# Optimization experiments

Measured on AMD Instinct MI355X. Metric: run time of the kernel, lower is better.

The kernel has to match this reference:

```python
import jax, jax.numpy as jnp
import numpy as np

B, S, D, H, DFF = 2, 4096, 512, 8, 2048
DK = D // H
EPS = 1e-5


def layer_norm(x, g, b):
    mu = jnp.mean(x, axis=-1, keepdims=True)
    var = jnp.mean((x - mu) ** 2, axis=-1, keepdims=True)
    return (x - mu) * jax.lax.rsqrt(var + EPS) * g + b


def setup_inputs() -> dict:
    key = jax.random.key(0)
    ks = jax.random.split(key, 12)
    s = 1.0 / np.sqrt(D)
    return {
        "x": jax.random.normal(ks[0], (B, S, D), jnp.float32),
        "mask": jnp.ones((B, 1, 1, S), jnp.int32),
        "wq": jax.random.normal(ks[1], (D, D), jnp.float32) * s,
        "wk": jax.random.normal(ks[2], (D, D), jnp.float32) * s,
        "wv": jax.random.normal(ks[3], (D, D), jnp.float32) * s,
        "wo": jax.random.normal(ks[4], (D, D), jnp.float32) * s,
        "w1": jax.random.normal(ks[5], (D, DFF), jnp.float32) * s,
        "b1": jnp.zeros((DFF,), jnp.float32),
        "w2": jax.random.normal(ks[6], (DFF, D), jnp.float32) * (1.0 / np.sqrt(DFF)),
        "b2": jnp.zeros((D,), jnp.float32),
        "g1": jnp.ones((D,), jnp.float32),
        "be1": jnp.zeros((D,), jnp.float32),
        "g2": jnp.ones((D,), jnp.float32),
        "be2": jnp.zeros((D,), jnp.float32),
    }


def reference(x, mask, wq, wk, wv, wo, w1, b1, w2, b2, g1, be1, g2, be2):
    # projections -> [B, H, S, DK]
    def split_heads(t):
        return t.reshape(B, S, H, DK).transpose(0, 2, 1, 3)

    q = split_heads(x @ wq)
    k = split_heads(x @ wk)
    v = split_heads(x @ wv)

    scores = jnp.einsum("bhqd,bhkd->bhqk", q, k) / np.sqrt(DK)
    scores = jnp.where(mask == 0, -1e9, scores)
    attn = jax.nn.softmax(scores, axis=-1)  # dropout=0 (eval)
    ctx = jnp.einsum("bhqk,bhkd->bhqd", attn, v)
    ctx = ctx.transpose(0, 2, 1, 3).reshape(B, S, D)
    attn_out = ctx @ wo

    x1 = layer_norm(x + attn_out, g1, be1)
    ff = jax.nn.relu(x1 @ w1 + b1) @ w2 + b2
    return layer_norm(x1 + ff, g2, be2)
```

## Files before the change

### kernel.cpp

```cpp
#include <hip/hip_runtime.h>
#include <hip/hip_bf16.h>


typedef unsigned short u16;
typedef unsigned int u32;
typedef __attribute__((ext_vector_type(2))) u32 u32x2;
typedef __attribute__((ext_vector_type(4))) u16 u16x4;
typedef __attribute__((ext_vector_type(8))) u16 u16x8;
typedef __attribute__((ext_vector_type(2))) float f32x2;
typedef __attribute__((ext_vector_type(4))) float f32x4;
typedef __attribute__((ext_vector_type(16))) float f32x16;
typedef __attribute__((ext_vector_type(8))) short bf16x8;

#define CB 2
#define CS 4096
#define CD 512
#define CH 8
#define CDK 64
#define CDFF 2048
#define NXC ((size_t)CB * CS * CD)
#define NSP 2
#define BH (CB * CH)
#define BHS (BH * CS)

__device__ __forceinline__ float bf2f(u16 u) {
    union { u32 i; float f; } c;
    c.i = ((u32)u) << 16;
    return c.f;
}

__device__ __forceinline__ u16 f2bf(float f) {
    u32 x = __float_as_uint(f);
    u32 r = (x + 0x7fffu + ((x >> 16) & 1u)) >> 16;
    return (u16)r;
}

__device__ __forceinline__ u32 packbf2(float a, float b) {
    __hip_bfloat162 h = __float22bfloat162_rn(float2{a, b});
    union { __hip_bfloat162 h; u32 u; } c;
    c.h = h;
    return c.u;
}

__device__ __forceinline__ void dma16(const u16* g, u16* l) {
    __builtin_amdgcn_global_load_lds(
        (const __attribute__((address_space(1))) void*)g,
        (__attribute__((address_space(3))) void*)l, 16, 0, 0);
}

__global__ void detect_dtype(const u32* __restrict__ xw, int* __restrict__ flag) {
    __shared__ int red[256];
    int sane = 0;
    for (int i = threadIdx.x; i < 2048; i += 256) {
        u32 w = xw[i];
        u32 lo = w & 0xFFFFu;
        u32 e = (lo >> 7) & 0xFFu;
        if (lo == 0u || lo == 0x8000u || (e >= 96u && e <= 159u)) sane++;
    }
    red[threadIdx.x] = sane;
    __syncthreads();
    for (int s = 128; s > 0; s >>= 1) {
        if ((int)threadIdx.x < s) red[threadIdx.x] += red[threadIdx.x + s];
        __syncthreads();
    }
    if (threadIdx.x == 0) *flag = (red[0] >= 1843) ? 1 : 0;
}

__global__ __launch_bounds__(256) void convert_bf16(
    const void* __restrict__ src, u16* __restrict__ dst, int n,
    const int* __restrict__ flag)
{
    const bool isbf = (*flag != 0);
    const int n8 = n >> 3;
    int i = blockIdx.x * 256 + threadIdx.x;
    const int stride = gridDim.x * 256;
    if (isbf) {
        const u16x8* s = (const u16x8*)src;
        u16x8* d = (u16x8*)dst;
        for (; i < n8; i += stride) d[i] = s[i];
    } else {
        const f32x4* s = (const f32x4*)src;
        for (; i < n8; i += stride) {
            f32x4 a = s[2 * i];
            f32x4 b = s[2 * i + 1];
            u16x8 o;
#pragma unroll
            for (int e = 0; e < 4; e++) {
                o[e] = f2bf(a[e]);
                o[4 + e] = f2bf(b[e]);
            }
            *(u16x8*)&dst[(size_t)i * 8] = o;
        }
    }
    if (blockIdx.x == 0 && threadIdx.x == 0) {
        for (int r = n8 * 8; r < n; r++) {
            if (isbf) dst[r] = ((const u16*)src)[r];
            else dst[r] = f2bf(((const float*)src)[r]);
        }
    }
}

struct SmallConv {
    const void* src[6];
    u16* dst[6];
    int n[6];
};

__global__ __launch_bounds__(256) void convert_small(SmallConv sc, const int* __restrict__ flag) {
    const bool isbf = (*flag != 0);
    for (int t = 0; t < 6; t++) {
        for (int i = threadIdx.x; i < sc.n[t]; i += 256) {
            if (isbf) sc.dst[t][i] = ((const u16*)sc.src[t])[i];
            else sc.dst[t][i] = f2bf(((const float*)sc.src[t])[i]);
        }
    }
}

__global__ __launch_bounds__(256) void build_mask_bits(
    const int* __restrict__ mask, unsigned long long* __restrict__ bits)
{
    int w = blockIdx.x * 4 + (threadIdx.x >> 6);
    int lane = threadIdx.x & 63;
    int b = w >> 6, t = w & 63;
    int val = mask[b * CS + t * 64 + lane];
    unsigned long long bal = __ballot(val != 0);
    if (lane == 0) bits[w] = bal;
}

__global__ __launch_bounds__(256) void transpose_cvt(
    const void* __restrict__ src, u16* __restrict__ dst,
    int R, int Cc, const int* __restrict__ flag)
{
    __shared__ float t[32][33];
    const bool isbf = (*flag != 0);
    const int r0 = blockIdx.y * 32;
    const int c0 = blockIdx.x * 32;
    const int col = threadIdx.x & 31;
    const int row = threadIdx.x >> 5;
#pragma unroll
    for (int it = 0; it < 4; it++) {
        int rr = row + it * 8;
        float v;
        if (isbf) v = bf2f(((const u16*)src)[(size_t)(r0 + rr) * Cc + c0 + col]);
        else v = ((const float*)src)[(size_t)(r0 + rr) * Cc + c0 + col];
        t[rr][col] = v;
    }
    __syncthreads();
#pragma unroll
    for (int it = 0; it < 4; it++) {
        int rr = row + it * 8;
        dst[(size_t)(c0 + rr) * R + r0 + col] = f2bf(t[col][rr]);
    }
}

#define F_SPLIT 1
#define F_BIAS  2
#define F_RELU  4

template <int FLAGS>
__global__ __launch_bounds__(256, 3) void gemm_mfma(
    const u16* __restrict__ A, const u16* __restrict__ Bt,
    const u16* __restrict__ bias, u16* __restrict__ C,
    int M, int N, int K)
{
    __shared__ u16 Asb[4096];
    __shared__ u16 Bsb[4096];

    const int tid = threadIdx.x;
    const int lane = tid & 63;
    const int wave = tid >> 6;
    const int lrow = lane & 15;
    const int quad = lane >> 4;
    const int wm = wave & 1;
    const int wn = wave >> 1;
    const int m0 = blockIdx.y * 128;
    const int n0 = blockIdx.x * 128;

    const int idx0 = wave * 128 + lane;
    const int idx1 = idx0 + 64;
    const u16* Ap0 = A + (size_t)(m0 + (idx0 >> 2)) * K + (idx0 & 3) * 8;
    const u16* Ap1 = A + (size_t)(m0 + (idx1 >> 2)) * K + (idx1 & 3) * 8;
    const u16* Bp0 = Bt + (size_t)(n0 + (idx0 >> 2)) * K + (idx0 & 3) * 8;
    const u16* Bp1 = Bt + (size_t)(n0 + (idx1 >> 2)) * K + (idx1 & 3) * 8;
    u16* Al0 = &Asb[wave * 1024];
    u16* Al1 = &Asb[wave * 1024 + 512];
    u16* Bl0 = &Bsb[wave * 1024];
    u16* Bl1 = &Bsb[wave * 1024 + 512];

    f32x4 acc[4][4];
#pragma unroll
    for (int i = 0; i < 4; i++)
#pragma unroll
        for (int j = 0; j < 4; j++) acc[i][j] = f32x4{0.f, 0.f, 0.f, 0.f};

    for (int k0 = 0; k0 < K; k0 += 32) {
        __syncthreads();
        dma16(Ap0 + k0, Al0);
        dma16(Ap1 + k0, Al1);
        dma16(Bp0 + k0, Bl0);
        dma16(Bp1 + k0, Bl1);
        __syncthreads();

        bf16x8 af[4], bfr[4];
#pragma unroll
        for (int i = 0; i < 4; i++)
            af[i] = *(const bf16x8*)&Asb[(wm * 64 + i * 16 + lrow) * 32 + quad * 8];
#pragma unroll
        for (int j = 0; j < 4; j++)
            bfr[j] = *(const bf16x8*)&Bsb[(wn * 64 + j * 16 + lrow) * 32 + quad * 8];
#pragma unroll
        for (int i = 0; i < 4; i++)
#pragma unroll
            for (int j = 0; j < 4; j++)
                acc[i][j] = __builtin_amdgcn_mfma_f32_16x16x32_bf16(
                    af[i], bfr[j], acc[i][j], 0, 0, 0);
    }

    const int mbase = m0 + wm * 64;
    const int nbase = n0 + wn * 64;
#pragma unroll
    for (int i = 0; i < 4; i++) {
#pragma unroll
        for (int j = 0; j < 4; j++) {
            const int n = nbase + j * 16 + lrow;
            if ((FLAGS & F_SPLIT) && ((nbase + j * 16) >> 9) == 2) {
                const int dk = n & 63;
                const int h = (n >> 6) & 7;
                const int sb = mbase + i * 16 + quad * 4;
                const int bb = sb >> 12;
                const int ss = sb & 4095;
                u16x4 ov;
#pragma unroll
                for (int r = 0; r < 4; r++) ov[r] = f2bf(acc[i][j][r]);
                *(u16x4*)&C[2 * NXC + (((size_t)(bb * CH + h)) * CDK + dk) * CS + ss] = ov;
            } else {
#pragma unroll
                for (int r = 0; r < 4; r++) {
                    const int m = mbase + i * 16 + quad * 4 + r;
                    float val = acc[i][j][r];
                    if (FLAGS & F_BIAS) val += bf2f(bias[n]);
                    if (FLAGS & F_RELU) val = fmaxf(val, 0.f);
                    if (FLAGS & F_SPLIT) {
                        const int proj = n >> 9;
                        const int d = n & 511;
                        const int h = d >> 6;
                        const int dk = d & 63;
                        const int bb = m >> 12;
                        const int ss = m & 4095;
                        C[proj * NXC + (((size_t)(bb * CH + h)) * CS + ss) * CDK + dk] = f2bf(val);
                    } else {
                        C[(size_t)m * N + n] = f2bf(val);
                    }
                }
            }
        }
    }
}

__global__ __launch_bounds__(256, 4) void mfma_attn2(
    const u16* __restrict__ Qb, const u16* __restrict__ Kb,
    const u16* __restrict__ Vt, const unsigned long long* __restrict__ bits,
    u16* __restrict__ pOT, float* __restrict__ Ls)
{
    __shared__ u16 KB[3][4096];
    __shared__ u16 VB[2][4096];

    const int tid = threadIdx.x;
    const int lane = tid & 63;
    const int wave = tid >> 6;
    const int qcol = lane & 31;
    const int hf = lane >> 5;

    const int bh = blockIdx.y;
    const int b = bh >> 3;
    const int z = blockIdx.z;
    const int q0 = blockIdx.x * 128 + wave * 32;

    const float SC = 0.125f * 1.44269504088896340736f;

    bf16x8 bq[4];
    const u16* qp = Qb + ((size_t)bh * CS + q0 + qcol) * CDK + hf * 8;
#pragma unroll
    for (int c = 0; c < 4; c++) {
        bf16x8 raw = *(const bf16x8*)(qp + c * 16);
        union { u32 u[4]; bf16x8 v; } cv;
#pragma unroll
        for (int j = 0; j < 4; j++)
            cv.u[j] = packbf2(bf2f((u16)raw[2 * j]) * SC, bf2f((u16)raw[2 * j + 1]) * SC);
        bq[c] = cv.v;
    }

    f32x4 z4 = {0.f, 0.f, 0.f, 0.f};
    asm volatile("" : "+v"(z4));
    f32x16 zero16;
#pragma unroll
    for (int i = 0; i < 16; i++) zero16[i] = z4[i & 3];

    f32x16 ot[2];
#pragma unroll
    for (int dt = 0; dt < 2; dt++)
#pragma unroll
        for (int i = 0; i < 16; i++) ot[dt][i] = 0.f;
    float lh = 0.f;

    const u16* kbase = Kb + (size_t)bh * CS * CDK;
    const u16* vbase = Vt + (size_t)bh * CDK * CS;
    const unsigned long long* bp = bits + b * 64;

    const int t0 = z * (CS / NSP);
    const int t1 = t0 + (CS / NSP);

    const int rsw = qcol & 7;
    int koff[2][4];
#pragma unroll
    for (int rt = 0; rt < 2; rt++)
#pragma unroll
        for (int c = 0; c < 4; c++)
            koff[rt][c] = ((rt * 32 + qcol) * 64 + (((2 * c + hf) ^ rsw) * 8)) * 2;
    const char* kb0 = (const char*)&KB[0][0];
    const char* vb0 = (const char*)&VB[0][0];

    const int w2 = wave * 2;

#define STAGE_K(KOFFB, t)                                                    \
    {                                                                        \
        const u16* kb_ = kbase + (size_t)(t) * CDK;                          \
        _Pragma("unroll")                                                    \
        for (int n = 0; n < 2; n++) {                                        \
            int idx = (w2 + n) * 64 + lane;                                  \
            int row = idx >> 3;                                              \
            int g = (idx & 7) ^ (row & 7);                                   \
            dma16(kb_ + row * CDK + g * 8,                                   \
                  (u16*)((char*)&KB[0][0] + (KOFFB) + (w2 + n) * 1024));     \
        }                                                                    \
    }
#define STAGE_V(P, t)                                                        \
    {                                                                        \
        const u16* vb_ = vbase + (t);                                        \
        _Pragma("unroll")                                                    \
        for (int n = 0; n < 2; n++) {                                        \
            int idx = (w2 + n) * 64 + lane;                                  \
            int row = idx >> 3;                                              \
            int g = (idx & 7) ^ (row & 7);                                   \
            dma16(vb_ + (size_t)row * CS + g * 8,                            \
                  (u16*)((char*)&VB[0][0] + (P) * 8192 + (w2 + n) * 1024));  \
        }                                                                    \
    }

#define TBODY(KROFF, VOFF, BM, MASKED, MIDSYNC)                              \
    {                                                                        \
        f32x2 racc = {0.f, 0.f};                                             \
        _Pragma("unroll")                                                    \
        for (int mt = 0; mt < 2; mt++) {                                     \
            f32x16 s;                                                        \
            _Pragma("unroll")                                                \
            for (int c = 0; c < 4; c++) {                                    \
                bf16x8 ak = *(const bf16x8*)(kb0 + (KROFF) + koff[mt][c]);   \
                s = __builtin_amdgcn_mfma_f32_32x32x16_bf16(                 \
                    ak, bq[c], (c == 0) ? zero16 : s, 0, 0, 0);              \
            }                                                                \
            if (MASKED) {                                                    \
                const unsigned long long bm_ = (BM);                         \
                if (bm_ != ~0ull) {                                          \
                    _Pragma("unroll")                                        \
                    for (int i = 0; i < 16; i++) {                           \
                        const int key = (i & 3) + 8 * (i >> 2) + 4 * hf + 32 * mt; \
                        if (!((bm_ >> key) & 1ull)) s[i] = -1e30f;           \
                    }                                                        \
                }                                                            \
            }                                                                \
            u32 pk[8];                                                       \
            _Pragma("unroll")                                                \
            for (int g = 0; g < 4; g++) {                                    \
                float p0 = __builtin_amdgcn_exp2f(s[4 * g + 0]);             \
                float p1 = __builtin_amdgcn_exp2f(s[4 * g + 1]);             \
                float p2 = __builtin_amdgcn_exp2f(s[4 * g + 2]);             \
                float p3 = __builtin_amdgcn_exp2f(s[4 * g + 3]);             \
                racc += f32x2{p0, p1};                                       \
                racc += f32x2{p2, p3};                                       \
                pk[2 * g + 0] = packbf2(p0, p1);                             \
                pk[2 * g + 1] = packbf2(p2, p3);                             \
            }                                                                \
            if (mt == 0) { MIDSYNC }                                         \
            _Pragma("unroll")                                                \
            for (int cc = 0; cc < 2; cc++) {                                 \
                u32x2 r0 = __builtin_amdgcn_permlane32_swap(                 \
                    pk[4 * cc + 0], pk[4 * cc + 2], false, false);           \
                u32x2 r1 = __builtin_amdgcn_permlane32_swap(                 \
                    pk[4 * cc + 1], pk[4 * cc + 3], false, false);           \
                union { u32 u[4]; bf16x8 v; } pf;                            \
                pf.u[0] = r0.x;                                              \
                pf.u[1] = r1.x;                                              \
                pf.u[2] = r0.y;                                              \
                pf.u[3] = r1.y;                                              \
                const int c = 2 * mt + cc;                                   \
                _Pragma("unroll")                                            \
                for (int dt = 0; dt < 2; dt++) {                             \
                    bf16x8 av = *(const bf16x8*)(vb0 + (VOFF) + koff[dt][c]); \
                    ot[dt] = __builtin_amdgcn_mfma_f32_32x32x16_bf16(        \
                        av, pf.v, ot[dt], 0, 0, 0);                          \
                }                                                            \
            }                                                                \
        }                                                                    \
        lh += racc.x + racc.y;                                               \
    }

#define FTILE(P, TT, KR, KS, DOV, DOK, TOPASM, MIDASM)                       \
    {                                                                        \
        asm volatile(TOPASM ::: "memory");                                   \
        __builtin_amdgcn_sched_barrier(0);                                   \
        __builtin_amdgcn_s_barrier();                                        \
        __builtin_amdgcn_sched_barrier(0);                                   \
        if (DOV) STAGE_V((P) ^ 1, (TT) + 64);                                \
        if (DOK) STAGE_K((KS), (TT) + 128);                                  \
        TBODY((KR), (P) * 8192, 0ull, 0,                                     \
              asm volatile(MIDASM ::: "memory");                             \
              __builtin_amdgcn_sched_barrier(0);                             \
              __builtin_amdgcn_s_barrier();                                  \
              __builtin_amdgcn_sched_barrier(0);)                            \
    }

    unsigned long long am = ~0ull;
    const int tb0 = t0 >> 6;
    for (int i = 0; i < 32; i++) am &= bp[tb0 + i];
    const bool allones = (am == ~0ull);

    if (allones) {
        STAGE_K(0, t0);
        STAGE_V(0, t0);
        STAGE_K(8192, t0 + 64);

        u32 kr = 0;
        for (int m = 0; m < 15; m++) {
            const int t = t0 + m * 128;
            const u32 kr1 = (kr == 16384u) ? 0u : kr + 8192u;
            const u32 ks0 = (kr1 == 16384u) ? 0u : kr1 + 8192u;
            FTILE(0, t, kr, ks0, 1, 1,
                  "s_waitcnt vmcnt(4)", "s_waitcnt vmcnt(6)")
            FTILE(1, t + 64, kr1, kr, 1, 1,
                  "s_waitcnt vmcnt(4)", "s_waitcnt vmcnt(6)")
            kr = ks0;
        }
        {
            const int t = t0 + 30 * 64;
            const u32 kr1 = (kr == 16384u) ? 0u : kr + 8192u;
            FTILE(0, t, kr, 0, 1, 0,
                  "s_waitcnt vmcnt(4)", "s_waitcnt vmcnt(4)")
            FTILE(1, t + 64, kr1, 0, 0, 0,
                  "s_waitcnt vmcnt(2)", "s_waitcnt vmcnt(0)")
        }
    } else {
        STAGE_K(0, t0);
        STAGE_V(0, t0);
        __syncthreads();
        for (int t = t0; t < t1; t += 64) {
            const int p = (t >> 6) & 1;
            const u32 kro = (u32)p * 8192u;
            if (t + 64 < t1) {
                STAGE_V(p ^ 1, t + 64);
                STAGE_K((p ^ 1) * 8192, t + 64);
            }
            TBODY(kro, p * 8192, bp[t >> 6], 1, ;)
            __syncthreads();
        }
    }
#undef FTILE
#undef TBODY
#undef STAGE_V
#undef STAGE_K

    u32x2 rr = __builtin_amdgcn_permlane32_swap(
        __float_as_uint(lh), __float_as_uint(lh), false, false);
    const float l = lh + __uint_as_float(hf ? rr.x : rr.y);

    const int q_lin = bh * CS + q0 + qcol;
    if (hf == 0) Ls[z * BHS + q_lin] = l;
    const size_t pbase = ((size_t)(z * BH + bh) * CDK) * CS + q0 + qcol;
#pragma unroll
    for (int dt = 0; dt < 2; dt++)
#pragma unroll
        for (int i = 0; i < 16; i++) {
            const int dk = (i & 3) + 8 * (i >> 2) + 4 * hf + 32 * dt;
            pOT[pbase + (size_t)dk * CS] = f2bf(ot[dt][i]);
        }
}

__global__ __launch_bounds__(256) void attn_combine(
    const u16* __restrict__ pOT, const float* __restrict__ Ls,
    u16* __restrict__ ctx)
{
    __shared__ float linv[64];
    __shared__ u16 T[64][72];

    const int bh = blockIdx.y;
    const int s0 = blockIdx.x * 64;
    const int b = bh >> 3, h = bh & 7;
    const int tid = threadIdx.x;

    if (tid < 64) {
        float L = 0.f;
#pragma unroll
        for (int z = 0; z < NSP; z++) L += Ls[z * BHS + bh * CS + s0 + tid];
        linv[tid] = (L > 0.f) ? 1.f / L : 0.f;
    }
    __syncthreads();

    const int dk = tid >> 2;
    const int sc = (tid & 3) * 16;
    float acc[16] = {};
#pragma unroll
    for (int z = 0; z < NSP; z++) {
        const u16* p = pOT + ((size_t)(z * BH + bh) * CDK + dk) * CS + s0 + sc;
        u16x8 v0 = *(const u16x8*)p;
        u16x8 v1 = *(const u16x8*)(p + 8);
#pragma unroll
        for (int e = 0; e < 8; e++) {
            acc[e] += bf2f(v0[e]);
            acc[8 + e] += bf2f(v1[e]);
        }
    }
#pragma unroll
    for (int e = 0; e < 16; e++)
        T[sc + e][dk] = f2bf(acc[e] * linv[sc + e]);
    __syncthreads();

    const int sr = tid >> 2;
    const int dc = (tid & 3) * 16;
    u16x8 o0, o1;
#pragma unroll
    for (int e = 0; e < 8; e++) {
        o0[e] = T[sr][dc + e];
        o1[e] = T[sr][dc + 8 + e];
    }
    u16* cp = &ctx[((size_t)b * CS + s0 + sr) * CD + h * CDK + dc];
    *(u16x8*)cp = o0;
    *(u16x8*)(cp + 8) = o1;
}

__global__ __launch_bounds__(256) void ln_kernel(
    const u16* __restrict__ xa, const u16* __restrict__ xb,
    const u16* __restrict__ g, const u16* __restrict__ be,
    u16* __restrict__ outb, float* __restrict__ outf,
    const int* __restrict__ flag)
{
    const int lane = threadIdx.x & 63;
    const int wave = threadIdx.x >> 6;
    const size_t row = (size_t)blockIdx.x * 4 + wave;
    const int c0 = lane * 8;

    u16x8 av = *(const u16x8*)(xa + row * CD + c0);
    u16x8 bv = *(const u16x8*)(xb + row * CD + c0);

    float v[8];
    float s1 = 0.f, s2 = 0.f;
#pragma unroll
    for (int e = 0; e < 8; e++) {
        v[e] = bf2f(av[e]) + bf2f(bv[e]);
        s1 += v[e];
        s2 += v[e] * v[e];
    }
#pragma unroll
    for (int off = 32; off > 0; off >>= 1) {
        s1 += __shfl_xor(s1, off, 64);
        s2 += __shfl_xor(s2, off, 64);
    }
    const float mu = s1 * (1.f / CD);
    const float var = fmaxf(s2 * (1.f / CD) - mu * mu, 0.f);
    const float r = rsqrtf(var + 1e-5f);

    u16x8 gv = *(const u16x8*)(g + c0);
    u16x8 ev = *(const u16x8*)(be + c0);
    float res[8];
#pragma unroll
    for (int e = 0; e < 8; e++)
        res[e] = (v[e] - mu) * r * bf2f(gv[e]) + bf2f(ev[e]);

    const int flg = *flag;
    const bool f32out = (outf != nullptr) && (flg == 0);
    if (f32out) {
        float4 o0 = make_float4(res[0], res[1], res[2], res[3]);
        float4 o1 = make_float4(res[4], res[5], res[6], res[7]);
        *(float4*)(outf + row * CD + c0) = o0;
        *(float4*)(outf + row * CD + c0 + 4) = o1;
    } else {
        u16x8 ov;
#pragma unroll
        for (int e = 0; e < 8; e++) ov[e] = f2bf(res[e]);
        *(u16x8*)(outb + row * CD + c0) = ov;
    }
}


extern "C" void kernel_launch(void* const* d_in, const int* in_sizes, int n_in,
                              void* d_out, int out_size, void* d_ws, size_t ws_size,
                              hipStream_t stream)
{
    const void* x_raw   = d_in[0];
    const int*  mask    = (const int*)d_in[1];
    const void* wq_raw  = d_in[2];
    const void* wk_raw  = d_in[3];
    const void* wv_raw  = d_in[4];
    const void* wo_raw  = d_in[5];
    const void* w1_raw  = d_in[6];
    const void* b1_raw  = d_in[7];
    const void* w2_raw  = d_in[8];
    const void* b2_raw  = d_in[9];
    const void* g1_raw  = d_in[10];
    const void* be1_raw = d_in[11];
    const void* g2_raw  = d_in[12];
    const void* be2_raw = d_in[13];

    const size_t NX = NXC;
    const size_t WSZ = (size_t)CD * CD;
    const size_t W1SZ = (size_t)CD * CDFF;

    u16* ws = (u16*)d_ws;
    int* flag = (int*)d_ws;
    unsigned long long* bits = (unsigned long long*)(ws + 512);
    u16* base = ws + 1024;
    u16* xc  = base;
    u16* q   = base + 1 * NX;
    u16* k   = base + 2 * NX;
    u16* v   = base + 3 * NX;
    u16* ctx = base + 4 * NX;
    u16* att = base + 5 * NX;
    u16* x1  = base + 6 * NX;
    u16* ffo = base + 7 * NX;
    u16* ffh = base + 8 * NX;
    u16* wt  = base + 12 * NX;
    u16* wqkvT = wt;
    u16* woT = wqkvT + 3 * WSZ;
    u16* w1T = woT + WSZ;
    u16* w2T = w1T + W1SZ;
    u16* b1c = w2T + W1SZ;
    u16* b2c = b1c + CDFF;
    u16* g1c = b2c + CD;
    u16* be1c = g1c + CD;
    u16* g2c = be1c + CD;
    u16* be2c = g2c + CD;
    u16* wend = be2c + CD;

    const size_t need = (size_t)(wend - ws) * sizeof(u16);
    if (ws_size < need) return;
    (void)k;

    u16* pOT = ffh;
    float* Ls = (float*)att;

    detect_dtype<<<1, 256, 0, stream>>>((const u32*)x_raw, flag);

    convert_bf16<<<1024, 256, 0, stream>>>(x_raw, xc, (int)NX, flag);
    build_mask_bits<<<32, 256, 0, stream>>>(mask, bits);

    transpose_cvt<<<dim3(CD / 32, CD / 32), 256, 0, stream>>>(wq_raw, wqkvT, CD, CD, flag);
    transpose_cvt<<<dim3(CD / 32, CD / 32), 256, 0, stream>>>(wk_raw, wqkvT + WSZ, CD, CD, flag);
    transpose_cvt<<<dim3(CD / 32, CD / 32), 256, 0, stream>>>(wv_raw, wqkvT + 2 * WSZ, CD, CD, flag);
    transpose_cvt<<<dim3(CD / 32, CD / 32), 256, 0, stream>>>(wo_raw, woT, CD, CD, flag);
    transpose_cvt<<<dim3(CDFF / 32, CD / 32), 256, 0, stream>>>(w1_raw, w1T, CD, CDFF, flag);
    transpose_cvt<<<dim3(CD / 32, CDFF / 32), 256, 0, stream>>>(w2_raw, w2T, CDFF, CD, flag);

    SmallConv sc;
    sc.src[0] = b1_raw;  sc.dst[0] = b1c;  sc.n[0] = CDFF;
    sc.src[1] = b2_raw;  sc.dst[1] = b2c;  sc.n[1] = CD;
    sc.src[2] = g1_raw;  sc.dst[2] = g1c;  sc.n[2] = CD;
    sc.src[3] = be1_raw; sc.dst[3] = be1c; sc.n[3] = CD;
    sc.src[4] = g2_raw;  sc.dst[4] = g2c;  sc.n[4] = CD;
    sc.src[5] = be2_raw; sc.dst[5] = be2c; sc.n[5] = CD;
    convert_small<<<1, 256, 0, stream>>>(sc, flag);

    const int M = CB * CS;

    gemm_mfma<F_SPLIT><<<dim3(1536 / 128, M / 128), 256, 0, stream>>>(
        xc, wqkvT, nullptr, q, M, 1536, CD);

    mfma_attn2<<<dim3(CS / 128, BH, NSP), 256, 0, stream>>>(q, k, v, bits, pOT, Ls);
    attn_combine<<<dim3(CS / 64, BH), 256, 0, stream>>>(pOT, Ls, ctx);

    gemm_mfma<0><<<dim3(CD / 128, M / 128), 256, 0, stream>>>(
        ctx, woT, nullptr, att, M, CD, CD);

    ln_kernel<<<dim3(M / 4), 256, 0, stream>>>(xc, att, g1c, be1c, x1, nullptr, flag);

    gemm_mfma<F_BIAS | F_RELU><<<dim3(CDFF / 128, M / 128), 256, 0, stream>>>(
        x1, w1T, b1c, ffh, M, CDFF, CD);
    gemm_mfma<F_BIAS><<<dim3(CD / 128, M / 128), 256, 0, stream>>>(
        ffh, w2T, b2c, ffo, M, CD, CDFF);

    ln_kernel<<<dim3(M / 4), 256, 0, stream>>>(x1, ffo, g2c, be2c,
                                               (u16*)d_out, (float*)d_out, flag);
}
```

Measured before the change: 339.2 us.

## Merge weight prep launches into one kernel and widen GEMM K-tile with swizzled LDS

The six transpose launches, the mask-bit build and the small-parameter conversion are folded into a single prep_all kernel that dispatches on block index, cutting per-launch overhead. Separately, the MFMA GEMM now stages a 64-wide K slice per iteration instead of 32, with an XOR swizzle on the 16-byte LDS chunk index. This halves the barrier count per K step and is meant to avoid LDS bank conflicts on the fragment reads. LDS per block doubles to 32 KB, which may affect occupancy at 3 blocks per CU.

```diff
diff --git a/kernel.cpp b/kernel.cpp
--- a/kernel.cpp
+++ b/kernel.cpp
@@ -100,56 +100,69 @@
     }
 }
 
-struct SmallConv {
-    const void* src[6];
-    u16* dst[6];
-    int n[6];
+struct PrepArgs {
+    const void* tsrc[6];
+    u16* tdst[6];
+    int R[6], Cc[6], nbx[6];
+    int cum[7];
+    const int* mask;
+    unsigned long long* bits;
+    const void* ssrc[6];
+    u16* sdst[6];
+    int sn[6];
 };
 
-__global__ __launch_bounds__(256) void convert_small(SmallConv sc, const int* __restrict__ flag) {
-    const bool isbf = (*flag != 0);
-    for (int t = 0; t < 6; t++) {
-        for (int i = threadIdx.x; i < sc.n[t]; i += 256) {
-            if (isbf) sc.dst[t][i] = ((const u16*)sc.src[t])[i];
-            else sc.dst[t][i] = f2bf(((const float*)sc.src[t])[i]);
-        }
-    }
-}
-
-__global__ __launch_bounds__(256) void build_mask_bits(
-    const int* __restrict__ mask, unsigned long long* __restrict__ bits)
-{
-    int w = blockIdx.x * 4 + (threadIdx.x >> 6);
-    int lane = threadIdx.x & 63;
-    int b = w >> 6, t = w & 63;
-    int val = mask[b * CS + t * 64 + lane];
-    unsigned long long bal = __ballot(val != 0);
-    if (lane == 0) bits[w] = bal;
-}
-
-__global__ __launch_bounds__(256) void transpose_cvt(
-    const void* __restrict__ src, u16* __restrict__ dst,
-    int R, int Cc, const int* __restrict__ flag)
-{
-    __shared__ float t[32][33];
-    const bool isbf = (*flag != 0);
-    const int r0 = blockIdx.y * 32;
-    const int c0 = blockIdx.x * 32;
-    const int col = threadIdx.x & 31;
-    const int row = threadIdx.x >> 5;
-#pragma unroll
-    for (int it = 0; it < 4; it++) {
-        int rr = row + it * 8;
-        float v;
-        if (isbf) v = bf2f(((const u16*)src)[(size_t)(r0 + rr) * Cc + c0 + col]);
-        else v = ((const float*)src)[(size_t)(r0 + rr) * Cc + c0 + col];
-        t[rr][col] = v;
-    }
-    __syncthreads();
-#pragma unroll
-    for (int it = 0; it < 4; it++) {
-        int rr = row + it * 8;
-        dst[(size_t)(c0 + rr) * R + r0 + col] = f2bf(t[col][rr]);
+__global__ __launch_bounds__(256) void prep_all(PrepArgs pa, const int* __restrict__ flag) {
+    const int bid = blockIdx.x;
+    const int tid = threadIdx.x;
+    if (bid < pa.cum[6]) {
+        __shared__ float t[32][33];
+        int w = 0;
+#pragma unroll
+        for (int k = 1; k < 6; k++) w += (bid >= pa.cum[k]) ? 1 : 0;
+        const int local = bid - pa.cum[w];
+        const int nbx = pa.nbx[w];
+        const int bx = local % nbx;
+        const int by = local / nbx;
+        const int R = pa.R[w];
+        const int Cc = pa.Cc[w];
+        const void* src = pa.tsrc[w];
+        u16* dst = pa.tdst[w];
+        const bool isbf = (*flag != 0);
+        const int r0 = by * 32;
+        const int c0 = bx * 32;
+        const int col = tid & 31;
+        const int row = tid >> 5;
+#pragma unroll
+        for (int it = 0; it < 4; it++) {
+            int rr = row + it * 8;
+            float v;
+            if (isbf) v = bf2f(((const u16*)src)[(size_t)(r0 + rr) * Cc + c0 + col]);
+            else v = ((const float*)src)[(size_t)(r0 + rr) * Cc + c0 + col];
+            t[rr][col] = v;
+        }
+        __syncthreads();
+#pragma unroll
+        for (int it = 0; it < 4; it++) {
+            int rr = row + it * 8;
+            dst[(size_t)(c0 + rr) * R + r0 + col] = f2bf(t[col][rr]);
+        }
+    } else if (bid < pa.cum[6] + 32) {
+        const int local = bid - pa.cum[6];
+        int w = local * 4 + (tid >> 6);
+        int lane = tid & 63;
+        int b = w >> 6, t = w & 63;
+        int val = pa.mask[b * CS + t * 64 + lane];
+        unsigned long long bal = __ballot(val != 0);
+        if (lane == 0) pa.bits[w] = bal;
+    } else {
+        const bool isbf = (*flag != 0);
+        for (int t = 0; t < 6; t++) {
+            for (int i = tid; i < pa.sn[t]; i += 256) {
+                if (isbf) pa.sdst[t][i] = ((const u16*)pa.ssrc[t])[i];
+                else pa.sdst[t][i] = f2bf(((const float*)pa.ssrc[t])[i]);
+            }
+        }
     }
 }
 
@@ -163,29 +176,34 @@
     const u16* __restrict__ bias, u16* __restrict__ C,
     int M, int N, int K)
 {
-    __shared__ u16 Asb[4096];
-    __shared__ u16 Bsb[4096];
+    __shared__ u16 AS[8192];
+    __shared__ u16 BS[8192];
 
     const int tid = threadIdx.x;
     const int lane = tid & 63;
     const int wave = tid >> 6;
     const int lrow = lane & 15;
     const int quad = lane >> 4;
+    const int rswg = lrow & 7;
     const int wm = wave & 1;
     const int wn = wave >> 1;
     const int m0 = blockIdx.y * 128;
     const int n0 = blockIdx.x * 128;
 
-    const int idx0 = wave * 128 + lane;
-    const int idx1 = idx0 + 64;
-    const u16* Ap0 = A + (size_t)(m0 + (idx0 >> 2)) * K + (idx0 & 3) * 8;
-    const u16* Ap1 = A + (size_t)(m0 + (idx1 >> 2)) * K + (idx1 & 3) * 8;
-    const u16* Bp0 = Bt + (size_t)(n0 + (idx0 >> 2)) * K + (idx0 & 3) * 8;
-    const u16* Bp1 = Bt + (size_t)(n0 + (idx1 >> 2)) * K + (idx1 & 3) * 8;
-    u16* Al0 = &Asb[wave * 1024];
-    u16* Al1 = &Asb[wave * 1024 + 512];
-    u16* Bl0 = &Bsb[wave * 1024];
-    u16* Bl1 = &Bsb[wave * 1024 + 512];
+    const u16* Aps[4];
+    const u16* Bps[4];
+    u16* Adst[4];
+    u16* Bdst[4];
+#pragma unroll
+    for (int r = 0; r < 4; r++) {
+        const int idx = r * 256 + tid;
+        const int row = idx >> 3;
+        const int g = (idx & 7) ^ (row & 7);
+        Aps[r] = A + (size_t)(m0 + row) * K + g * 8;
+        Bps[r] = Bt + (size_t)(n0 + row) * K + g * 8;
+        Adst[r] = &AS[r * 2048 + wave * 512];
+        Bdst[r] = &BS[r * 2048 + wave * 512];
+    }
 
     f32x4 acc[4][4];
 #pragma unroll
@@ -193,27 +211,40 @@
 #pragma unroll
         for (int j = 0; j < 4; j++) acc[i][j] = f32x4{0.f, 0.f, 0.f, 0.f};
 
-    for (int k0 = 0; k0 < K; k0 += 32) {
+    const char* As8 = (const char*)&AS[0];
+    const char* Bs8 = (const char*)&BS[0];
+
+    for (int k0 = 0; k0 < K; k0 += 64) {
         __syncthreads();
-        dma16(Ap0 + k0, Al0);
-        dma16(Ap1 + k0, Al1);
-        dma16(Bp0 + k0, Bl0);
-        dma16(Bp1 + k0, Bl1);
+#pragma unroll
+        for (int r = 0; r < 4; r++) {
+            dma16(Aps[r] + k0, Adst[r]);
+            dma16(Bps[r] + k0, Bdst[r]);
+        }
         __syncthreads();
 
-        bf16x8 af[4], bfr[4];
-#pragma unroll
-        for (int i = 0; i < 4; i++)
-            af[i] = *(const bf16x8*)&Asb[(wm * 64 + i * 16 + lrow) * 32 + quad * 8];
-#pragma unroll
-        for (int j = 0; j < 4; j++)
-            bfr[j] = *(const bf16x8*)&Bsb[(wn * 64 + j * 16 + lrow) * 32 + quad * 8];
-#pragma unroll
-        for (int i = 0; i < 4; i++)
-#pragma unroll
-            for (int j = 0; j < 4; j++)
-                acc[i][j] = __builtin_amdgcn_mfma_f32_16x16x32_bf16(
-                    af[i], bfr[j], acc[i][j], 0, 0, 0);
+#pragma unroll
+        for (int kk = 0; kk < 2; kk++) {
+            bf16x8 af[4], bfr[4];
+#pragma unroll
+            for (int i = 0; i < 4; i++) {
+                const int row = wm * 64 + i * 16 + lrow;
+                af[i] = *(const bf16x8*)(As8 + row * 128 +
+                                         (((kk * 4 + quad) ^ rswg) << 4));
+            }
+#pragma unroll
+            for (int j = 0; j < 4; j++) {
+                const int row = wn * 64 + j * 16 + lrow;
+                bfr[j] = *(const bf16x8*)(Bs8 + row * 128 +
+                                          (((kk * 4 + quad) ^ rswg) << 4));
+            }
+#pragma unroll
+            for (int i = 0; i < 4; i++)
+#pragma unroll
+                for (int j = 0; j < 4; j++)
+                    acc[i][j] = __builtin_amdgcn_mfma_f32_16x16x32_bf16(
+                        af[i], bfr[j], acc[i][j], 0, 0, 0);
+        }
     }
 
     const int mbase = m0 + wm * 64;
@@ -650,23 +681,30 @@
     detect_dtype<<<1, 256, 0, stream>>>((const u32*)x_raw, flag);
 
     convert_bf16<<<1024, 256, 0, stream>>>(x_raw, xc, (int)NX, flag);
-    build_mask_bits<<<32, 256, 0, stream>>>(mask, bits);
-
-    transpose_cvt<<<dim3(CD / 32, CD / 32), 256, 0, stream>>>(wq_raw, wqkvT, CD, CD, flag);
-    transpose_cvt<<<dim3(CD / 32, CD / 32), 256, 0, stream>>>(wk_raw, wqkvT + WSZ, CD, CD, flag);
-    transpose_cvt<<<dim3(CD / 32, CD / 32), 256, 0, stream>>>(wv_raw, wqkvT + 2 * WSZ, CD, CD, flag);
-    transpose_cvt<<<dim3(CD / 32, CD / 32), 256, 0, stream>>>(wo_raw, woT, CD, CD, flag);
-    transpose_cvt<<<dim3(CDFF / 32, CD / 32), 256, 0, stream>>>(w1_raw, w1T, CD, CDFF, flag);
-    transpose_cvt<<<dim3(CD / 32, CDFF / 32), 256, 0, stream>>>(w2_raw, w2T, CDFF, CD, flag);
-
-    SmallConv sc;
-    sc.src[0] = b1_raw;  sc.dst[0] = b1c;  sc.n[0] = CDFF;
-    sc.src[1] = b2_raw;  sc.dst[1] = b2c;  sc.n[1] = CD;
-    sc.src[2] = g1_raw;  sc.dst[2] = g1c;  sc.n[2] = CD;
-    sc.src[3] = be1_raw; sc.dst[3] = be1c; sc.n[3] = CD;
-    sc.src[4] = g2_raw;  sc.dst[4] = g2c;  sc.n[4] = CD;
-    sc.src[5] = be2_raw; sc.dst[5] = be2c; sc.n[5] = CD;
-    convert_small<<<1, 256, 0, stream>>>(sc, flag);
+
+    PrepArgs pa;
+    pa.tsrc[0] = wq_raw; pa.tdst[0] = wqkvT;           pa.R[0] = CD;   pa.Cc[0] = CD;
+    pa.tsrc[1] = wk_raw; pa.tdst[1] = wqkvT + WSZ;     pa.R[1] = CD;   pa.Cc[1] = CD;
+    pa.tsrc[2] = wv_raw; pa.tdst[2] = wqkvT + 2 * WSZ; pa.R[2] = CD;   pa.Cc[2] = CD;
+    pa.tsrc[3] = wo_raw; pa.tdst[3] = woT;             pa.R[3] = CD;   pa.Cc[3] = CD;
+    pa.tsrc[4] = w1_raw; pa.tdst[4] = w1T;             pa.R[4] = CD;   pa.Cc[4] = CDFF;
+    pa.tsrc[5] = w2_raw; pa.tdst[5] = w2T;             pa.R[5] = CDFF; pa.Cc[5] = CD;
+    int cum = 0;
+    for (int w = 0; w < 6; w++) {
+        pa.nbx[w] = pa.Cc[w] / 32;
+        pa.cum[w] = cum;
+        cum += (pa.Cc[w] / 32) * (pa.R[w] / 32);
+    }
+    pa.cum[6] = cum;
+    pa.mask = mask;
+    pa.bits = bits;
+    pa.ssrc[0] = b1_raw;  pa.sdst[0] = b1c;  pa.sn[0] = CDFF;
+    pa.ssrc[1] = b2_raw;  pa.sdst[1] = b2c;  pa.sn[1] = CD;
+    pa.ssrc[2] = g1_raw;  pa.sdst[2] = g1c;  pa.sn[2] = CD;
+    pa.ssrc[3] = be1_raw; pa.sdst[3] = be1c; pa.sn[3] = CD;
+    pa.ssrc[4] = g2_raw;  pa.sdst[4] = g2c;  pa.sn[4] = CD;
+    pa.ssrc[5] = be2_raw; pa.sdst[5] = be2c; pa.sn[5] = CD;
+    prep_all<<<cum + 32 + 1, 256, 0, stream>>>(pa, flag);
 
     const int M = CB * CS;
 
```

Measured after the change: 315.6 us. -6.9%, faster.
